# Kernel optimization log

Hardware: AMD Instinct MI355X
Metric: run time of the kernel (lower is better)

## Reference

```python
import jax, jax.numpy as jnp
import numpy as np

DIM = 128      # matrix dimension of the positional maps
N = 1024       # number of unique tree positions
MAX_POS = 65536  # positions < 2^16 -> path length <= 15 bits
L = 16         # static number of scan steps (covers max path length)


def setup_inputs() -> dict:
    key = jax.random.key(0)
    k1, k2 = jax.random.split(key)
    # replicate torch init: rand(2,d,d).softmax(-1).cumsum(-1)
    u = jax.random.uniform(k1, (2, DIM, DIM), dtype=jnp.float32)
    primitives = jnp.cumsum(jax.nn.softmax(u, axis=-1), axis=-1)
    unique = jax.random.randint(k2, (N,), 0, MAX_POS, dtype=jnp.int64)
    return {"unique": unique, "primitives": primitives}


def reference(unique, primitives):
    dtype = primitives.dtype
    dim = primitives.shape[-1]
    # hermitian = P - P^H (real -> skew-symmetric); primitives = matrix_exp(hermitian)
    herm = primitives - jnp.swapaxes(primitives, -1, -2)          # [2, d, d]
    expP = jax.vmap(jax.scipy.linalg.expm)(herm)                  # [2, d, d]
    eye = jnp.eye(dim, dtype=dtype)
    # linear(x, W) = x @ W.T ; word==2 (padding / exhausted path) applies identity
    trans = jnp.stack([expP[0].T, expP[1].T, eye])                # [3, d, d]

    # pos_to_path: bits of pos, LSB-first, dropping the leading 1.
    # bit at step s is (pos >> s) & 1, valid while (pos >> s) >= 2; pos<=1 -> empty path.
    steps = jnp.arange(L, dtype=unique.dtype)
    shifted = unique[None, :] >> steps[:, None]                   # [L, N]
    words = jnp.where(shifted >= 2, shifted & 1, 2)               # [L, N] in {0,1,2}

    def step(maps, w):
        # maps[n] <- maps[n] @ trans[w[n]]   (sequential composition along the path)
        return jnp.einsum('nij,njk->nik', maps, trans[w]), None

    maps0 = jnp.broadcast_to(eye, (unique.shape[0], dim, dim))    # identity.repeat(N,1,1)
    maps, _ = jax.lax.scan(step, maps0, words)
    return maps
```

## Files before the change

kernel.cpp:

```cpp
#include <hip/hip_runtime.h>

typedef unsigned int uint32;
typedef unsigned short u16;
typedef __attribute__((ext_vector_type(8))) short bf16x8;
typedef __attribute__((ext_vector_type(4))) float f32x4;
typedef __attribute__((ext_vector_type(2))) uint32 u32x2;
typedef __attribute__((ext_vector_type(4))) uint32 u32x4;

#define DIM 128
#define MAT (DIM * DIM)
#define GR  2048
#define PLANE 16384
#define MFMA __builtin_amdgcn_mfma_f32_16x16x32_bf16


__device__ __forceinline__ u16 f2bf(float x) {
    uint32 u = __float_as_uint(x);
    u += 0x7fffu + ((u >> 16) & 1u);
    return (u16)(u >> 16);
}
__device__ __forceinline__ float bf2f(u16 h) { return __uint_as_float(((uint32)h) << 16); }
__device__ __forceinline__ void split2(float x, u16& a0, u16& a1) {
    a0 = f2bf(x); a1 = f2bf(x - bf2f(a0));
}
__device__ __forceinline__ uint32 pack2(u16 a, u16 b) { return (uint32)a | ((uint32)b << 16); }
__device__ __forceinline__ uint4 packu4(const u16 (&a)[8]) {
    uint4 v; v.x = pack2(a[0], a[1]); v.y = pack2(a[2], a[3]);
    v.z = pack2(a[4], a[5]); v.w = pack2(a[6], a[7]); return v;
}
__device__ __forceinline__ uint32 comp4(const uint4& v, int c) {
    return c == 0 ? v.x : c == 1 ? v.y : c == 2 ? v.z : v.w;
}
__device__ __forceinline__ void transp8(const uint4 (&in)[8], uint4 (&out)[8]) {
#pragma unroll
    for (int c = 0; c < 8; ++c) {
        u16 o[8];
#pragma unroll
        for (int k = 0; k < 8; ++k) o[k] = (u16)(comp4(in[k], c >> 1) >> ((c & 1) * 16));
        out[c].x = pack2(o[0], o[1]); out[c].y = pack2(o[2], o[3]);
        out[c].z = pack2(o[4], o[5]); out[c].w = pack2(o[6], o[7]);
    }
}

template<bool PBLDS, int NP>
__device__ __forceinline__ void mm2(const uint4* __restrict__ pah, const uint4* __restrict__ pal,
                                    const uint4* __restrict__ pbh, const uint4* __restrict__ pbl,
                                    f32x4 (&acc)[4][4]) {
    const int tid = threadIdx.x, lane = tid & 63, w = tid >> 6;
    const int wr = (w >> 1) * 64, wc = (w & 1) * 64, lr = lane & 15, lg = lane >> 4;
#pragma unroll 1
    for (int kb = 0; kb < 4; ++kb) {
        const int g = kb * 4 + lg;
        bf16x8 ah[4], al[4], bh[4], bl[4];
#pragma unroll
        for (int t = 0; t < 4; ++t) {
            int ra = wr + t * 16 + lr;
            ah[t] = *(const bf16x8*)&pah[g * 128 + ra];
            if (NP == 3) al[t] = *(const bf16x8*)&pal[g * 128 + ra];
            int rb = wc + t * 16 + lr;
            int ib = PBLDS ? (rb * 16 + (g ^ (rb & 7))) : (g * 128 + rb);
            bh[t] = *(const bf16x8*)&pbh[ib];
            if (NP == 3) bl[t] = *(const bf16x8*)&pbl[ib];
        }
#pragma unroll
        for (int i = 0; i < 4; ++i)
#pragma unroll
            for (int j = 0; j < 4; ++j) {
                acc[i][j] = MFMA(ah[i], bh[j], acc[i][j], 0, 0, 0);
                if (NP == 3) {
                    acc[i][j] = MFMA(ah[i], bl[j], acc[i][j], 0, 0, 0);
                    acc[i][j] = MFMA(al[i], bh[j], acc[i][j], 0, 0, 0);
                }
            }
    }
}

__device__ __forceinline__ void acc_to_lds2(const f32x4 (&acc)[4][4], uint4* Mh, uint4* Ml) {
    const int tid = threadIdx.x, lane = tid & 63, w = tid >> 6;
    const int wr = (w >> 1) * 64, wc = (w & 1) * 64, lr = lane & 15, lg = lane >> 4;
#pragma unroll
    for (int i = 0; i < 4; ++i) {
        int u0 = wr + i * 16 + 4 * lg, half = (u0 >> 2) & 1, gq = u0 >> 3;
#pragma unroll
        for (int j = 0; j < 4; ++j) {
            int m = wc + j * 16 + lr;
            u16 h[4], l[4];
#pragma unroll
            for (int q = 0; q < 4; ++q) split2(acc[i][j][q], h[q], l[q]);
            uint2 hv; hv.x = pack2(h[0], h[1]); hv.y = pack2(h[2], h[3]);
            uint2 lv; lv.x = pack2(l[0], l[1]); lv.y = pack2(l[2], l[3]);
            int base = m * 16 + (gq ^ (m & 7));
            ((uint2*)&Mh[base])[half] = hv;
            ((uint2*)&Ml[base])[half] = lv;
        }
    }
}

__device__ __forceinline__ void acc_to_gN(const f32x4 (&acc)[4][4], uint4* nh, uint4* nl) {
    const int tid = threadIdx.x, lane = tid & 63, w = tid >> 6;
    const int wr = (w >> 1) * 64, wc = (w & 1) * 64, lr = lane & 15, lg = lane >> 4;
#pragma unroll
    for (int i = 0; i < 4; ++i) {
        int u0 = wr + i * 16 + 4 * lg, half = (u0 >> 2) & 1, gq = u0 >> 3;
#pragma unroll
        for (int j = 0; j < 4; ++j) {
            int m = wc + j * 16 + lr;
            u16 h[4], l[4];
#pragma unroll
            for (int q = 0; q < 4; ++q) split2(acc[i][j][q], h[q], l[q]);
            uint2 hv; hv.x = pack2(h[0], h[1]); hv.y = pack2(h[2], h[3]);
            uint2 lv; lv.x = pack2(l[0], l[1]); lv.y = pack2(l[2], l[3]);
            int base = gq * 128 + m;
            ((uint2*)&nh[base])[half] = hv;
            ((uint2*)&nl[base])[half] = lv;
        }
    }
}

__device__ __forceinline__ void acc_to_out(const f32x4 (&acc)[4][4], float* O) {
    const int tid = threadIdx.x, lane = tid & 63, w = tid >> 6;
    const int wr = (w >> 1) * 64, wc = (w & 1) * 64, lr = lane & 15, lg = lane >> 4;
#pragma unroll
    for (int i = 0; i < 4; ++i) {
        int u0 = wr + i * 16 + 4 * lg;
#pragma unroll
        for (int j = 0; j < 4; ++j) {
            int m = wc + j * 16 + lr;
            *(f32x4*)&O[m * DIM + u0] = acc[i][j];
        }
    }
}

__device__ __forceinline__ void mm2w(const uint4* __restrict__ pah, const uint4* __restrict__ pal,
                                     const uint4* __restrict__ pbh, const uint4* __restrict__ pbl,
                                     f32x4 (&acc)[2][2]) {
    const int tid = threadIdx.x, lane = tid & 63, w = tid >> 6;
    const int wr = (w >> 2) * 32, wc = (w & 3) * 32, lr = lane & 15, lg = lane >> 4;
#pragma unroll 1
    for (int kb = 0; kb < 4; ++kb) {
        const int g = kb * 4 + lg;
        bf16x8 ah[2], al[2], bh[2], bl[2];
#pragma unroll
        for (int t = 0; t < 2; ++t) {
            int ra = wr + t * 16 + lr;
            ah[t] = *(const bf16x8*)&pah[g * 128 + ra];
            al[t] = *(const bf16x8*)&pal[g * 128 + ra];
            int rb = wc + t * 16 + lr;
            int ib = rb * 16 + (g ^ (rb & 7));
            bh[t] = *(const bf16x8*)&pbh[ib];
            bl[t] = *(const bf16x8*)&pbl[ib];
        }
#pragma unroll
        for (int i = 0; i < 2; ++i)
#pragma unroll
            for (int j = 0; j < 2; ++j) {
                acc[i][j] = MFMA(ah[i], bh[j], acc[i][j], 0, 0, 0);
                acc[i][j] = MFMA(ah[i], bl[j], acc[i][j], 0, 0, 0);
                acc[i][j] = MFMA(al[i], bh[j], acc[i][j], 0, 0, 0);
            }
    }
}
__device__ __forceinline__ void acc_to_lds2w(const f32x4 (&acc)[2][2], uint4* Mh, uint4* Ml) {
    const int tid = threadIdx.x, lane = tid & 63, w = tid >> 6;
    const int wr = (w >> 2) * 32, wc = (w & 3) * 32, lr = lane & 15, lg = lane >> 4;
#pragma unroll
    for (int i = 0; i < 2; ++i) {
        int u0 = wr + i * 16 + 4 * lg, half = (u0 >> 2) & 1, gq = u0 >> 3;
#pragma unroll
        for (int j = 0; j < 2; ++j) {
            int m = wc + j * 16 + lr;
            u16 h[4], l[4];
#pragma unroll
            for (int q = 0; q < 4; ++q) split2(acc[i][j][q], h[q], l[q]);
            uint2 hv; hv.x = pack2(h[0], h[1]); hv.y = pack2(h[2], h[3]);
            uint2 lv; lv.x = pack2(l[0], l[1]); lv.y = pack2(l[2], l[3]);
            int base = m * 16 + (gq ^ (m & 7));
            ((uint2*)&Mh[base])[half] = hv;
            ((uint2*)&Ml[base])[half] = lv;
        }
    }
}

__device__ __forceinline__ void stage_lds(const uint4* sh, const uint4* sl, uint4* Mh, uint4* Ml) {
    for (int s = threadIdx.x; s < GR; s += blockDim.x) {
        int g = s >> 7, row = s & 127;
        int d = row * 16 + (g ^ (row & 7));
        Mh[d] = sh[s]; Ml[d] = sl[s];
    }
}
__device__ __forceinline__ void copyN(const uint4* Mh, const uint4* Ml, uint4* dh, uint4* dl) {
    for (int s2 = threadIdx.x; s2 < 2 * GR; s2 += blockDim.x) {
        const uint4* src = (s2 & GR) ? Ml : Mh;
        uint4* dst = (s2 & GR) ? dl : dh;
        int s = s2 & (GR - 1);
        int g = s >> 7, row = s & 127;
        dst[s] = src[row * 16 + (g ^ (row & 7))];
    }
}
__device__ __forceinline__ void copyT(const uint4* Mh, const uint4* Ml, uint4* dh, uint4* dl) {
    for (int tk = threadIdx.x; tk < 512; tk += blockDim.x) {
        const uint4* src = (tk & 256) ? Ml : Mh;
        uint4* dst = (tk & 256) ? dl : dh;
        int t = tk & 255, br = t >> 4, bc = t & 15;
        uint4 in[8], out[8];
#pragma unroll
        for (int k = 0; k < 8; ++k) { int r = br * 8 + k; in[k] = src[r * 16 + (bc ^ (r & 7))]; }
        transp8(in, out);
#pragma unroll
        for (int k = 0; k < 8; ++k) dst[br * 128 + bc * 8 + k] = out[k];
    }
}


__device__ __forceinline__ void wlds2s(u16* dst, int m, int u0, f32x4 v) {
    u16 a0[4], a1[4];
#pragma unroll
    for (int q = 0; q < 4; ++q) split2(v[q], a0[q], a1[q]);
    int e = ((m >> 2) * 8 + (u0 >> 4)) * 64 + (m & 3) * 16 + (u0 & 15);
    uint2 w0; w0.x = pack2(a0[0], a0[1]); w0.y = pack2(a0[2], a0[3]);
    uint2 w1; w1.x = pack2(a1[0], a1[1]); w1.y = pack2(a1[2], a1[3]);
    *(uint2*)&dst[0 * PLANE + e] = w0;
    *(uint2*)&dst[1 * PLANE + e] = w1;
}

template<bool ATR>
__device__ __forceinline__ void mmS(const uint4* __restrict__ pa, const u16* __restrict__ XSu,
                                    f32x4 (&acc)[2][4], int wr, int wc, int lr, int lg) {
#pragma unroll
    for (int i = 0; i < 2; ++i)
#pragma unroll
        for (int j = 0; j < 4; ++j) { f32x4 z = {0.f, 0.f, 0.f, 0.f}; acc[i][j] = z; }
    const uint32 lds_base = (uint32)(size_t)(const void*)XSu;
#pragma unroll 1
    for (int kb = 0; kb < 4; ++kb) {
        const int g = kb * 4 + lg;
        u32x2 t0[2][2], t1[2][2];
        bf16x8 aa[2][2], bb[4][2];
        if (ATR) {
#pragma unroll
            for (int t = 0; t < 2; ++t) {
                uint32 ba = lds_base + (uint32)(((16 * g + (wr >> 4) + t) << 7) + 8 * lr);
#pragma unroll
                for (int sp = 0; sp < 2; ++sp) {
                    asm volatile("ds_read_b64_tr_b16 %0, %2\n\t"
                                 "ds_read_b64_tr_b16 %1, %2 offset:1024"
                                 : "=&v"(t0[t][sp]), "=&v"(t1[t][sp])
                                 : "v"(ba + (uint32)(sp * 2 * PLANE)));
                }
            }
        } else {
#pragma unroll
            for (int t = 0; t < 2; ++t) {
                int ra = wr + t * 16 + lr;
#pragma unroll
                for (int sp = 0; sp < 2; ++sp) aa[t][sp] = *(const bf16x8*)&pa[sp * GR + g * 128 + ra];
            }
        }
#pragma unroll
        for (int t = 0; t < 4; ++t) {
            int rb = wc + t * 16 + lr;
            int e = ((rb >> 2) * 8 + (g >> 1)) * 64 + (rb & 3) * 16 + (g & 1) * 8;
#pragma unroll
            for (int sp = 0; sp < 2; ++sp) bb[t][sp] = *(const bf16x8*)&XSu[sp * PLANE + e];
        }
        if (ATR) {
            asm volatile("s_waitcnt lgkmcnt(0)" ::: "memory");
            __builtin_amdgcn_sched_barrier(0);
#pragma unroll
            for (int t = 0; t < 2; ++t)
#pragma unroll
                for (int sp = 0; sp < 2; ++sp) {
                    u32x4 v; v.x = t0[t][sp].x; v.y = t0[t][sp].y;
                    v.z = t1[t][sp].x; v.w = t1[t][sp].y;
                    aa[t][sp] = *(bf16x8*)&v;
                }
        }
#pragma unroll
        for (int i = 0; i < 2; ++i)
#pragma unroll
            for (int j = 0; j < 4; ++j) {
                acc[i][j] = MFMA(aa[i][0], bb[j][0], acc[i][j], 0, 0, 0);
                acc[i][j] = MFMA(aa[i][0], bb[j][1], acc[i][j], 0, 0, 0);
                acc[i][j] = MFMA(aa[i][1], bb[j][0], acc[i][j], 0, 0, 0);
            }
    }
}

__global__ __launch_bounds__(512) void expm_kernel(
        const float* __restrict__ P, float* __restrict__ NBf, float* __restrict__ NB2f,
        u16* TBp, u16* TB3p,
        u16* TThp, u16* TTlp, u16* TNhp, u16* TNlp) {
    __shared__ uint4 XL[4 * GR];
    u16* XSu = (u16*)XL;
    u16* PR0 = XSu;
    u16* PR1 = XSu + 2 * PLANE;
    const int b = blockIdx.x, tid = threadIdx.x;
    const int lane = tid & 63, w = tid >> 6;
    const int wr = (w >> 1) * 32, wc = (w & 1) * 64, lr = lane & 15, lg = lane >> 4;
    const float* Pm = P + b * MAT;
    float* nbf = NBf + b * MAT;
    float* nb2f = NB2f + b * MAT;
    uint4* tb  = (uint4*)TBp  + (size_t)b * 3 * GR;
    uint4* tb3 = (uint4*)TB3p + (size_t)b * 3 * GR;
    uint4* TTh = (uint4*)TThp; uint4* TTl = (uint4*)TTlp;
    uint4* TNh = (uint4*)TNhp; uint4* TNl = (uint4*)TNlp;

    const float C6f = 1.0f / 720.0f, C7f = 1.0f / 5040.0f, C8f = 1.0f / 40320.0f, C9f = 1.0f / 362880.0f;

    for (int s = tid; s < GR; s += 512) {
        int r = s >> 4, g = s & 15;
        float vv[8];
#pragma unroll
        for (int k = 0; k < 8; ++k) {
            int c = g * 8 + k;
            vv[k] = (Pm[r * DIM + c] - Pm[c * DIM + r]) * (1.0f / 32.0f);
        }
        float4 f0; f0.x = vv[0]; f0.y = vv[1]; f0.z = vv[2]; f0.w = vv[3];
        float4 f1; f1.x = vv[4]; f1.y = vv[5]; f1.z = vv[6]; f1.w = vv[7];
        *(float4*)&nbf[r * DIM + g * 8] = f0;
        *(float4*)&nbf[r * DIM + g * 8 + 4] = f1;
        u16 s0[8], s1[8];
#pragma unroll
        for (int k = 0; k < 8; ++k) split2(vv[k], s0[k], s1[k]);
        int d = ((r >> 2) * 8 + (g >> 1)) * 64 + (r & 3) * 16 + (g & 1) * 8;
        *(uint4*)&PR0[0 * PLANE + d] = packu4(s0);
        *(uint4*)&PR0[1 * PLANE + d] = packu4(s1);
#pragma unroll
        for (int k = 0; k < 8; ++k) { s0[k] ^= 0x8000; s1[k] ^= 0x8000; }
        int gi = g * 128 + r;
        tb[0 * GR + gi] = packu4(s0); tb[1 * GR + gi] = packu4(s1);
    }
    __syncthreads();

    f32x4 acc[2][4];

    mmS<true>(nullptr, PR0, acc, wr, wc, lr, lg);
#pragma unroll
    for (int i = 0; i < 2; ++i) { int u0 = wr + i * 16 + 4 * lg;
#pragma unroll
        for (int j = 0; j < 4; ++j) { int m = wc + j * 16 + lr;
            *(f32x4*)&nb2f[m * DIM + u0] = acc[i][j];
            wlds2s(PR1, m, u0, acc[i][j]);
        } }
    __syncthreads();

    mmS<false>(tb, PR1, acc, wr, wc, lr, lg);
#pragma unroll
    for (int i = 0; i < 2; ++i) { int u0 = wr + i * 16 + 4 * lg; int half = (u0 >> 2) & 1; int gi = (u0 >> 3) * 128;
#pragma unroll
        for (int j = 0; j < 4; ++j) { int m = wc + j * 16 + lr;
            f32x4 a = acc[i][j];
            u16 a0[4], a1[4];
#pragma unroll
            for (int q = 0; q < 4; ++q) split2(-a[q], a0[q], a1[q]);
            uint2 w0; w0.x = pack2(a0[0], a0[1]); w0.y = pack2(a0[2], a0[3]);
            uint2 w1; w1.x = pack2(a1[0], a1[1]); w1.y = pack2(a1[2], a1[3]);
            ((uint2*)&tb3[0 * GR + gi + m])[half] = w0;
            ((uint2*)&tb3[1 * GR + gi + m])[half] = w1;
            f32x4 bv = *(const f32x4*)&nbf[m * DIM + u0];
            f32x4 b2v = *(const f32x4*)&nb2f[m * DIM + u0];
            f32x4 x0;
#pragma unroll
            for (int q = 0; q < 4; ++q)
                x0[q] = a[q] * C9f + b2v[q] * C8f + bv[q] * C7f + ((u0 + q == m) ? C6f : 0.0f);
            wlds2s(PR0, m, u0, x0);
        } }
    __syncthreads();

    mmS<false>(tb3, PR0, acc, wr, wc, lr, lg);
#pragma unroll
    for (int i = 0; i < 2; ++i) { int u0 = wr + i * 16 + 4 * lg;
#pragma unroll
        for (int j = 0; j < 4; ++j) { int m = wc + j * 16 + lr;
            f32x4 bv = *(const f32x4*)&nbf[m * DIM + u0];
            f32x4 b2v = *(const f32x4*)&nb2f[m * DIM + u0];
            f32x4 x1;
#pragma unroll
            for (int q = 0; q < 4; ++q)
                x1[q] = acc[i][j][q] + bv[q] * (1.0f / 24.0f) + b2v[q] * (1.0f / 120.0f)
                      + ((u0 + q == m) ? (1.0f / 6.0f) : 0.0f);
            wlds2s(PR1, m, u0, x1);
        } }
    __syncthreads();

    mmS<false>(tb3, PR1, acc, wr, wc, lr, lg);
#pragma unroll
    for (int i = 0; i < 2; ++i) { int u0 = wr + i * 16 + 4 * lg;
#pragma unroll
        for (int j = 0; j < 4; ++j) { int m = wc + j * 16 + lr;
            f32x4 bv = *(const f32x4*)&nbf[m * DIM + u0];
            f32x4 b2v = *(const f32x4*)&nb2f[m * DIM + u0];
            f32x4 x2;
#pragma unroll
            for (int q = 0; q < 4; ++q)
                x2[q] = acc[i][j][q] + bv[q] + b2v[q] * 0.5f + ((u0 + q == m) ? 1.0f : 0.0f);
            wlds2s(PR0, m, u0, x2);
        } }
    __syncthreads();

    for (int sq = 0; sq < 5; ++sq) {
        const u16* src = (sq & 1) ? PR1 : PR0;
        u16* dst = (sq & 1) ? PR0 : PR1;
        mmS<true>(nullptr, src, acc, wr, wc, lr, lg);
        if (sq < 4) {
#pragma unroll
            for (int i = 0; i < 2; ++i) { int u0 = wr + i * 16 + 4 * lg;
#pragma unroll
                for (int j = 0; j < 4; ++j) wlds2s(dst, wc + j * 16 + lr, u0, acc[i][j]);
            }
            __syncthreads();
        } else {
#pragma unroll
            for (int i = 0; i < 2; ++i) { int u0 = wr + i * 16 + 4 * lg; int half = (u0 >> 2) & 1;
#pragma unroll
                for (int j = 0; j < 4; ++j) { int m = wc + j * 16 + lr;
                    u16 h[4], l[4];
#pragma unroll
                    for (int q = 0; q < 4; ++q) split2(acc[i][j][q], h[q], l[q]);
                    uint2 hv; hv.x = pack2(h[0], h[1]); hv.y = pack2(h[2], h[3]);
                    uint2 lv; lv.x = pack2(l[0], l[1]); lv.y = pack2(l[2], l[3]);
                    int base = m * 16 + ((u0 >> 3) ^ (m & 7));
                    ((uint2*)&XL[2 * GR + base])[half] = hv;
                    ((uint2*)&XL[3 * GR + base])[half] = lv;
                } }
            __syncthreads();
            copyN(XL + 2 * GR, XL + 3 * GR, TTh + (size_t)b * GR, TTl + (size_t)b * GR);
            copyT(XL + 2 * GR, XL + 3 * GR, TNh + (size_t)b * GR, TNl + (size_t)b * GR);
        }
    }
}

__global__ __launch_bounds__(1024) void chain_kernel(u16* TThp, u16* TTlp, u16* TNhp, u16* TNlp,
                                                     int schemeA) {
    __shared__ uint4 Mh[GR], Ml[GR];
    uint4* TTh = (uint4*)TThp; uint4* TTl = (uint4*)TTlp;
    uint4* TNh = (uint4*)TNhp; uint4* TNl = (uint4*)TNlp;
    int b = blockIdx.x;
    if (b == 28) {
        int id = schemeA ? 274 : 126;
        for (int s = threadIdx.x; s < GR; s += 1024) {
            int g = s >> 7, row = s & 127;
            u16 h[8];
#pragma unroll
            for (int k = 0; k < 8; ++k) h[k] = (g * 8 + k == row) ? (u16)0x3F80 : (u16)0;
            TNh[(size_t)id * GR + s] = packu4(h);
            uint4 z; z.x = z.y = z.z = z.w = 0u;
            TNl[(size_t)id * GR + s] = z;
        }
        return;
    }
    int v = 4 + b;
    int nb = 31 - __clz(v);
    int b0 = v & 1;
    stage_lds(TNh + (size_t)b0 * GR, TNl + (size_t)b0 * GR, Mh, Ml);
    __syncthreads();
    for (int t = 1; t < nb; ++t) {
        int bt = (v >> t) & 1;
        f32x4 acc[2][2] = {};
        mm2w(TTh + (size_t)bt * GR, TTl + (size_t)bt * GR, Mh, Ml, acc);
        __syncthreads();
        acc_to_lds2w(acc, Mh, Ml);
        __syncthreads();
    }
    copyT(Mh, Ml, TTh + (size_t)(v - 2) * GR, TTl + (size_t)(v - 2) * GR);
    bool needN = schemeA ? (v >= 16) : true;
    if (needN) {
        int tn = schemeA ? (v - 14) : (v - 2);
        copyN(Mh, Ml, TNh + (size_t)tn * GR, TNl + (size_t)tn * GR);
    }
}

__global__ __launch_bounds__(256) void pair_kernel(u16* TThp, u16* TTlp, u16* TNhp, u16* TNlp,
                                                   int schemeA) {
    extern __shared__ uint4 PL[];
    uint4* TTh = (uint4*)TThp; uint4* TTl = (uint4*)TTlp;
    uint4* TNh = (uint4*)TNhp; uint4* TNl = (uint4*)TNlp;
    int v = 32 + blockIdx.x;
    int c4 = v & 15;
    int tnb = schemeA ? (2 + c4) : (14 + c4);
    int tta = (v >> 4) - 2;
    if (schemeA) {
        f32x4 acc[4][4] = {};
        if (v < 256) {
            mm2<false, 3>(TNh + (size_t)tnb * GR, TNl + (size_t)tnb * GR,
                          TTh + (size_t)tta * GR, TTl + (size_t)tta * GR, acc);
            acc_to_gN(acc, TTh + (size_t)(v - 2) * GR, TTl + (size_t)(v - 2) * GR);
        } else {
            mm2<false, 3>(TTh + (size_t)tta * GR, TTl + (size_t)tta * GR,
                          TNh + (size_t)tnb * GR, TNl + (size_t)tnb * GR, acc);
            int tn = 18 + (v - 256);
            acc_to_gN(acc, TNh + (size_t)tn * GR, TNl + (size_t)tn * GR);
        }
    } else {
        f32x4 acc[4][4] = {};
        mm2<false, 3>(TTh + (size_t)tta * GR, TTl + (size_t)tta * GR,
                      TNh + (size_t)tnb * GR, TNl + (size_t)tnb * GR, acc);
        acc_to_gN(acc, TNh + (size_t)(v - 2) * GR, TNl + (size_t)(v - 2) * GR);
        acc_to_lds2(acc, PL, PL + GR);
        __syncthreads();
        copyT(PL, PL + GR, TTh + (size_t)(v - 2) * GR, TTl + (size_t)(v - 2) * GR);
    }
}

__global__ __launch_bounds__(256) void final_kernel(const u16* TThp, const u16* TTlp,
                                                    const u16* TNhp, const u16* TNlp,
                                                    const int* __restrict__ uq,
                                                    float* __restrict__ out, int schemeA) {
    extern __shared__ uint4 FL[];
    const uint4* TTh = (const uint4*)TThp; const uint4* TTl = (const uint4*)TTlp;
    const uint4* TNh = (const uint4*)TNhp; const uint4* TNl = (const uint4*)TNlp;
    float* O = out + (size_t)blockIdx.x * MAT;
    unsigned p = (unsigned)uq[blockIdx.x];

    if (p < 2u) {
        for (int s = threadIdx.x; s < 4096; s += 256) {
            int r = s >> 5, c0 = (s & 31) * 4;
            float4 v; v.x = v.y = v.z = v.w = 0.f;
            int d = r - c0;
            if (d == 0) v.x = 1.f; else if (d == 1) v.y = 1.f;
            else if (d == 2) v.z = 1.f; else if (d == 3) v.w = 1.f;
            *(float4*)&O[r * DIM + c0] = v;
        }
        return;
    }

    const uint4 *pah, *pal, *pbh, *pbl;
    int m3 = -1;
    if (schemeA) {
        const int id = 274;
        if (p < 256u) {
            pah = TTh + (size_t)(p - 2) * GR; pal = TTl + (size_t)(p - 2) * GR;
            pbh = TNh + (size_t)id * GR;      pbl = TNl + (size_t)id * GR;
        } else {
            int lo = (int)(p & 255u); unsigned hi = p >> 8;
            pbh = TNh + (size_t)(18 + lo) * GR; pbl = TNl + (size_t)(18 + lo) * GR;
            if (hi >= 2u) { pah = TTh + (size_t)(hi - 2) * GR; pal = TTl + (size_t)(hi - 2) * GR; }
            else          { pah = TNh + (size_t)id * GR;       pal = TNl + (size_t)id * GR; }
        }
        f32x4 acc[4][4] = {};
        mm2<false, 1>(pah, pal, pbh, pbl, acc);
        acc_to_out(acc, O);
        return;
    }
    {
        int f[3]; int m = 0; unsigned q = p;
        while (q >= 128u) { f[m++] = 64 + (int)(q & 63u); q >>= 6; }
        f[m++] = (int)q;
        if (m == 1) {
            const uint4* sh = TNh + (size_t)(f[0] - 2) * GR;
            const uint4* sl = TNl + (size_t)(f[0] - 2) * GR;
            for (int s = threadIdx.x; s < GR; s += 256) {
                int row = s >> 4, g = s & 15;
                uint4 H = sh[g * 128 + row], L = sl[g * 128 + row];
                float4 o0, o1;
                o0.x = bf2f((u16)(H.x & 0xffff)) + bf2f((u16)(L.x & 0xffff));
                o0.y = bf2f((u16)(H.x >> 16))    + bf2f((u16)(L.x >> 16));
                o0.z = bf2f((u16)(H.y & 0xffff)) + bf2f((u16)(L.y & 0xffff));
                o0.w = bf2f((u16)(H.y >> 16))    + bf2f((u16)(L.y >> 16));
                o1.x = bf2f((u16)(H.z & 0xffff)) + bf2f((u16)(L.z & 0xffff));
                o1.y = bf2f((u16)(H.z >> 16))    + bf2f((u16)(L.z >> 16));
                o1.z = bf2f((u16)(H.w & 0xffff)) + bf2f((u16)(L.w & 0xffff));
                o1.w = bf2f((u16)(H.w >> 16))    + bf2f((u16)(L.w >> 16));
                *(float4*)&O[row * DIM + g * 8] = o0;
                *(float4*)&O[row * DIM + g * 8 + 4] = o1;
            }
            return;
        }
        pbh = TNh + (size_t)(f[0] - 2) * GR; pbl = TNl + (size_t)(f[0] - 2) * GR;
        pah = TTh + (size_t)(f[1] - 2) * GR; pal = TTl + (size_t)(f[1] - 2) * GR;
        if (m == 3) m3 = f[2] - 2;
    }

    f32x4 acc[4][4] = {};
    mm2<false, 3>(pah, pal, pbh, pbl, acc);
    if (m3 < 0) { acc_to_out(acc, O); return; }
    acc_to_lds2(acc, FL, FL + GR);
    __syncthreads();
    f32x4 a2[4][4] = {};
    mm2<true, 3>(TTh + (size_t)m3 * GR, TTl + (size_t)m3 * GR, FL, FL + GR, a2);
    acc_to_out(a2, O);
}

extern "C" void kernel_launch(void* const* d_in, const int* in_sizes, int n_in,
                              void* d_out, int out_size, void* d_ws, size_t ws_size,
                              hipStream_t stream) {
    const int*   uq = (const int*)d_in[0];
    const float* P  = (const float*)d_in[1];
    float* out = (float*)d_out;

    const size_t needA = (size_t)(2 * 254 + 2 * 275 + 18) * MAT * 2 + (size_t)4 * MAT * 4;
    const bool A = ws_size >= needA;
    const int nTT = A ? 254 : 126;
    const int nTN = A ? 275 : 127;

    u16* TTh = (u16*)d_ws;
    u16* TTl = TTh + (size_t)nTT * MAT;
    u16* TNh = TTl + (size_t)nTT * MAT;
    u16* TNl = TNh + (size_t)nTN * MAT;
    u16* TB  = TNl + (size_t)nTN * MAT;
    u16* TB3 = TB  + (size_t)6 * MAT;
    u16* XTg = TB3 + (size_t)6 * MAT;
    float* NBf  = (float*)(XTg + (size_t)6 * MAT);
    float* NB2f = NBf + 2 * MAT;

    expm_kernel<<<2, 512, 0, stream>>>(P, NBf, NB2f, TB, TB3, TTh, TTl, TNh, TNl);
    chain_kernel<<<29, 1024, 0, stream>>>(TTh, TTl, TNh, TNl, (int)A);
    pair_kernel<<<A ? 480 : 96, 256, A ? 0 : 65536, stream>>>(TTh, TTl, TNh, TNl, (int)A);
    final_kernel<<<1024, 256, A ? 0 : 65536, stream>>>(TTh, TTl, TNh, TNl, uq, out, (int)A);
}
```

Baseline: 104.1 us.

## Replace serial chain kernel with two parallel level kernels; store hi-only pair outputs

In scheme A, the single 29-block chain kernel that built the small precomputed transition products is replaced by two kernels (9 blocks, then 40 blocks). Each block computes one 128x128 product, so the dependency chain becomes two wide levels instead of sequential work inside large blocks. The pair kernel now writes only the high bf16 part of its results, dropping the low-part split and store. This cuts global writes, but it only holds if later consumers never read those low parts, and it adds one more kernel launch.

```diff
diff --git a/kernel.cpp b/kernel.cpp
--- a/kernel.cpp
+++ b/kernel.cpp
@@ -113,6 +113,23 @@
             int base = gq * 128 + m;
             ((uint2*)&nh[base])[half] = hv;
             ((uint2*)&nl[base])[half] = lv;
+        }
+    }
+}
+__device__ __forceinline__ void acc_to_gN1(const f32x4 (&acc)[4][4], uint4* nh) {
+    const int tid = threadIdx.x, lane = tid & 63, w = tid >> 6;
+    const int wr = (w >> 1) * 64, wc = (w & 1) * 64, lr = lane & 15, lg = lane >> 4;
+#pragma unroll
+    for (int i = 0; i < 4; ++i) {
+        int u0 = wr + i * 16 + 4 * lg, half = (u0 >> 2) & 1, gq = u0 >> 3;
+#pragma unroll
+        for (int j = 0; j < 4; ++j) {
+            int m = wc + j * 16 + lr;
+            u16 h[4];
+#pragma unroll
+            for (int q = 0; q < 4; ++q) h[q] = f2bf(acc[i][j][q]);
+            uint2 hv; hv.x = pack2(h[0], h[1]); hv.y = pack2(h[2], h[3]);
+            ((uint2*)&nh[gq * 128 + m])[half] = hv;
         }
     }
 }
@@ -430,6 +447,68 @@
     }
 }
 
+__device__ __forceinline__ uint4* nv4h_p(u16* XTgp, u16* TBp, int i) {
+    return i < 3 ? (uint4*)XTgp + (size_t)(2 * i) * GR : (uint4*)TBp + (size_t)2 * GR;
+}
+__device__ __forceinline__ uint4* nv4l_p(u16* XTgp, u16* TBp, int i) {
+    return i < 3 ? (uint4*)XTgp + (size_t)(2 * i + 1) * GR : (uint4*)TBp + (size_t)5 * GR;
+}
+
+__global__ __launch_bounds__(256) void levelA_kernel(u16* TThp, u16* TTlp, u16* TNhp, u16* TNlp,
+                                                     u16* XTgp, u16* TBp) {
+    uint4* TTh = (uint4*)TThp; uint4* TTl = (uint4*)TTlp;
+    uint4* TNh = (uint4*)TNhp; uint4* TNl = (uint4*)TNlp;
+    int b = blockIdx.x;
+    if (b == 8) {
+        for (int s = threadIdx.x; s < GR; s += 256) {
+            int g = s >> 7, row = s & 127;
+            u16 h[8];
+#pragma unroll
+            for (int k = 0; k < 8; ++k) h[k] = (g * 8 + k == row) ? (u16)0x3F80 : (u16)0;
+            TNh[(size_t)274 * GR + s] = packu4(h);
+            uint4 z; z.x = z.y = z.z = z.w = 0u;
+            TNl[(size_t)274 * GR + s] = z;
+        }
+        return;
+    }
+    int c = 4 + (b & 3);
+    int b0 = c & 1, b1 = (c >> 1) & 1;
+    f32x4 acc[4][4] = {};
+    if (b < 4) {
+        mm2<false, 3>(TNh + (size_t)b0 * GR, TNl + (size_t)b0 * GR,
+                      TTh + (size_t)b1 * GR, TTl + (size_t)b1 * GR, acc);
+        acc_to_gN(acc, TTh + (size_t)(c - 2) * GR, TTl + (size_t)(c - 2) * GR);
+    } else {
+        mm2<false, 3>(TTh + (size_t)b1 * GR, TTl + (size_t)b1 * GR,
+                      TNh + (size_t)b0 * GR, TNl + (size_t)b0 * GR, acc);
+        acc_to_gN(acc, nv4h_p(XTgp, TBp, b - 4), nv4l_p(XTgp, TBp, b - 4));
+    }
+}
+
+__global__ __launch_bounds__(256) void levelB_kernel(u16* TThp, u16* TTlp, u16* TNhp, u16* TNlp,
+                                                     u16* XTgp, u16* TBp) {
+    uint4* TTh = (uint4*)TThp; uint4* TTl = (uint4*)TTlp;
+    uint4* TNh = (uint4*)TNhp; uint4* TNl = (uint4*)TNlp;
+    int b = blockIdx.x;
+    f32x4 acc[4][4] = {};
+    if (b < 8) {
+        int i = b;
+        mm2<false, 3>(TNh + (size_t)(i & 1) * GR, TNl + (size_t)(i & 1) * GR,
+                      TTh + (size_t)(2 + (i >> 1)) * GR, TTl + (size_t)(2 + (i >> 1)) * GR, acc);
+        acc_to_gN(acc, TTh + (size_t)(6 + i) * GR, TTl + (size_t)(6 + i) * GR);
+    } else if (b < 24) {
+        int i = b - 8;
+        mm2<false, 3>(nv4h_p(XTgp, TBp, i & 3), nv4l_p(XTgp, TBp, i & 3),
+                      TTh + (size_t)(2 + (i >> 2)) * GR, TTl + (size_t)(2 + (i >> 2)) * GR, acc);
+        acc_to_gN(acc, TTh + (size_t)(14 + i) * GR, TTl + (size_t)(14 + i) * GR);
+    } else {
+        int i = b - 24;
+        mm2<false, 3>(TTh + (size_t)(2 + (i >> 2)) * GR, TTl + (size_t)(2 + (i >> 2)) * GR,
+                      nv4h_p(XTgp, TBp, i & 3), nv4l_p(XTgp, TBp, i & 3), acc);
+        acc_to_gN(acc, TNh + (size_t)(2 + i) * GR, TNl + (size_t)(2 + i) * GR);
+    }
+}
+
 __global__ __launch_bounds__(1024) void chain_kernel(u16* TThp, u16* TTlp, u16* TNhp, u16* TNlp,
                                                      int schemeA) {
     __shared__ uint4 Mh[GR], Ml[GR];
@@ -484,12 +563,11 @@
         if (v < 256) {
             mm2<false, 3>(TNh + (size_t)tnb * GR, TNl + (size_t)tnb * GR,
                           TTh + (size_t)tta * GR, TTl + (size_t)tta * GR, acc);
-            acc_to_gN(acc, TTh + (size_t)(v - 2) * GR, TTl + (size_t)(v - 2) * GR);
+            acc_to_gN1(acc, TTh + (size_t)(v - 2) * GR);
         } else {
             mm2<false, 3>(TTh + (size_t)tta * GR, TTl + (size_t)tta * GR,
                           TNh + (size_t)tnb * GR, TNl + (size_t)tnb * GR, acc);
-            int tn = 18 + (v - 256);
-            acc_to_gN(acc, TNh + (size_t)tn * GR, TNl + (size_t)tn * GR);
+            acc_to_gN1(acc, TNh + (size_t)(18 + (v - 256)) * GR);
         }
     } else {
         f32x4 acc[4][4] = {};
@@ -604,7 +682,12 @@
     float* NB2f = NBf + 2 * MAT;
 
     expm_kernel<<<2, 512, 0, stream>>>(P, NBf, NB2f, TB, TB3, TTh, TTl, TNh, TNl);
-    chain_kernel<<<29, 1024, 0, stream>>>(TTh, TTl, TNh, TNl, (int)A);
+    if (A) {
+        levelA_kernel<<<9, 256, 0, stream>>>(TTh, TTl, TNh, TNl, XTg, TB);
+        levelB_kernel<<<40, 256, 0, stream>>>(TTh, TTl, TNh, TNl, XTg, TB);
+    } else {
+        chain_kernel<<<29, 1024, 0, stream>>>(TTh, TTl, TNh, TNl, 0);
+    }
     pair_kernel<<<A ? 480 : 96, 256, A ? 0 : 65536, stream>>>(TTh, TTl, TNh, TNl, (int)A);
     final_kernel<<<1024, 256, A ? 0 : 65536, stream>>>(TTh, TTl, TNh, TNl, uq, out, (int)A);
 }
```

New measurement: 103.5 us. About the same (-0.6%).
